# Performance work log

Hardware: AMD Instinct MI355X
Metric: run time of the kernel (lower is better)

## Reference

```python
import jax, jax.numpy as jnp
import numpy as np

EPS = 1e-08

def setup_inputs() -> dict:
    key = jax.random.key(0)
    kq, kk, kv = jax.random.split(key, 3)
    B, H, S, D = 2, 16, 2048, 64
    q = jax.random.normal(kq, (B, H, S, D), dtype=jnp.float32)
    k = jax.random.normal(kk, (B, H, S, D), dtype=jnp.float32)
    v = jax.random.normal(kv, (B, H, S, D), dtype=jnp.float32)
    return {"q": q, "k": k, "v": v}

def reference(q, k, v):
    d_k = q.shape[-1]
    # scores: [B,H,S,S]
    scores = jnp.einsum('bhqd,bhkd->bhqk', q, k) / jnp.sqrt(jnp.asarray(d_k, q.dtype))
    attn_weights = jax.nn.softmax(scores, axis=-1)
    # output: [B,H,S,D]
    output = jnp.einsum('bhqk,bhkd->bhqd', attn_weights, v)
    # non-differentiable row-norm preconditioner C_ii = 1/||A[i]||_2
    row_norms = jnp.linalg.norm(jax.lax.stop_gradient(output), axis=-1, keepdims=True)
    preconditioned_output = output / (row_norms + EPS)
    return (preconditioned_output, attn_weights)
```

## Files before the change

### kernel.cpp

```cpp
#include <hip/hip_runtime.h>

#define SS 2048
#define DD 64
#define S2 0.18033688011112042f

typedef __attribute__((ext_vector_type(4))) float f32x4;
typedef __attribute__((ext_vector_type(8))) short bfx8;
typedef __attribute__((ext_vector_type(4))) short bfx4;

__device__ __forceinline__ short f2bf(float f) {
    unsigned u = __builtin_bit_cast(unsigned, f);
    u += 0x7fffu + ((u >> 16) & 1u);
    return (short)(u >> 16);
}
__device__ __forceinline__ bfx8 pack8(f32x4 a, f32x4 b) {
    bfx8 r;
    r[0] = f2bf(a[0]); r[1] = f2bf(a[1]); r[2] = f2bf(a[2]); r[3] = f2bf(a[3]);
    r[4] = f2bf(b[0]); r[5] = f2bf(b[1]); r[6] = f2bf(b[2]); r[7] = f2bf(b[3]);
    return r;
}
__device__ __forceinline__ float bf2f(short s) {
    unsigned u = ((unsigned)(unsigned short)s) << 16;
    return __builtin_bit_cast(float, u);
}
__device__ __forceinline__ void bar_raw() {
    asm volatile("s_barrier" ::: "memory");
    __builtin_amdgcn_sched_barrier(0);
}
__device__ __forceinline__ void wait_vm0() {
    asm volatile("s_waitcnt vmcnt(0)" ::: "memory");
    __builtin_amdgcn_sched_barrier(0);
}
__device__ __forceinline__ void wait_vm2() {
    asm volatile("s_waitcnt vmcnt(2)" ::: "memory");
    __builtin_amdgcn_sched_barrier(0);
}
__device__ __forceinline__ void wait_vm8() {
    asm volatile("s_waitcnt vmcnt(8)" ::: "memory");
    __builtin_amdgcn_sched_barrier(0);
}
__device__ __forceinline__ void gload16(const void* g, void* l) {
    __builtin_amdgcn_global_load_lds(
        (const __attribute__((address_space(1))) unsigned*)g,
        (__attribute__((address_space(3))) unsigned*)l, 16, 0, 0);
}

__global__ __launch_bounds__(256) void prep_kernel(
    const float* __restrict__ k, const float* __restrict__ v,
    short* __restrict__ kbf, short* __restrict__ vtbf)
{
    const int blk = blockIdx.x;
    const int bh = blk >> 4, kc = blk & 15;
    const int tid = threadIdx.x;
    const long hoff = (long)bh * SS * DD;

    {
        const int key = tid >> 1, h = tid & 1;
        const float* kp = k + hoff + (long)(kc * 128 + key) * DD + h * 32;
        char* krow = (char*)kbf + ((long)bh * SS + kc * 128 + key) * 128;
        const int x = (key & 3) << 5;
        #pragma unroll
        for (int i = 0; i < 4; ++i) {
            f32x4 a = *(const f32x4*)(kp + i * 8);
            f32x4 b = *(const f32x4*)(kp + i * 8 + 4);
            *(bfx8*)(krow + ((h * 64 + i * 16) ^ x)) = pack8(a, b);
        }
    }

    __shared__ __align__(16) short Vl[64][136];
    {
        const int kq = (tid & 31) * 4, dg = (tid >> 5) * 8;
        const float* vp = v + hoff + (long)(kc * 128 + kq) * DD + dg;
        f32x4 r0a = *(const f32x4*)(vp),        r0b = *(const f32x4*)(vp + 4);
        f32x4 r1a = *(const f32x4*)(vp + DD),   r1b = *(const f32x4*)(vp + DD + 4);
        f32x4 r2a = *(const f32x4*)(vp + 2*DD), r2b = *(const f32x4*)(vp + 2*DD + 4);
        f32x4 r3a = *(const f32x4*)(vp + 3*DD), r3b = *(const f32x4*)(vp + 3*DD + 4);
        #pragma unroll
        for (int d = 0; d < 4; ++d) {
            bfx4 w;
            w[0] = f2bf(r0a[d]); w[1] = f2bf(r1a[d]);
            w[2] = f2bf(r2a[d]); w[3] = f2bf(r3a[d]);
            *(bfx4*)&Vl[dg + d][kq] = w;
        }
        #pragma unroll
        for (int d = 0; d < 4; ++d) {
            bfx4 w;
            w[0] = f2bf(r0b[d]); w[1] = f2bf(r1b[d]);
            w[2] = f2bf(r2b[d]); w[3] = f2bf(r3b[d]);
            *(bfx4*)&Vl[dg + 4 + d][kq] = w;
        }
    }
    __syncthreads();
    {
        const int d = tid >> 2, quar = tid & 3;
        char* vrow = (char*)vtbf + ((long)bh * 64 + d) * 4096 + kc * 256;
        const int x = (d & 3) << 5;
        #pragma unroll
        for (int i = 0; i < 4; ++i) {
            bfx8 w = *(const bfx8*)((const char*)&Vl[d][0] + quar * 64 + i * 16);
            *(bfx8*)(vrow + ((quar * 64 + i * 16) ^ x)) = w;
        }
    }
}

__global__ __launch_bounds__(256, 2) void pattn_main2(
    const float* __restrict__ q, const short* __restrict__ kbf,
    const short* __restrict__ vtbf, float* __restrict__ out,
    float* __restrict__ attn)
{
    const int blk = blockIdx.x;
    const int bh  = (blk & 7) * 4 + ((blk >> 3) & 3);
    const int qt  = blk >> 5;
    const int tid = threadIdx.x;
    const int wid = tid >> 6, lane = tid & 63;
    const int c = lane & 15, g = lane >> 4;

    __shared__ __align__(16) short Kl[2][64][64];
    __shared__ __align__(16) short Vt[2][64][64];
    __shared__ __align__(16) short Wc[4][32][80];

    const long hoff = (long)bh * SS * DD;
    const int  qA = qt * 128 + wid * 32 + c;
    const int  qB = qA + 16;

    bfx8 bqA0, bqA1, bqB0, bqB1;
    {
        const float* qp = q + hoff + (long)qA * DD + 8 * g;
        bqA0 = pack8(*(const f32x4*)(qp)      * S2, *(const f32x4*)(qp + 4)  * S2);
        bqA1 = pack8(*(const f32x4*)(qp + 32) * S2, *(const f32x4*)(qp + 36) * S2);
        const float* qp2 = q + hoff + (long)qB * DD + 8 * g;
        bqB0 = pack8(*(const f32x4*)(qp2)      * S2, *(const f32x4*)(qp2 + 4)  * S2);
        bqB1 = pack8(*(const f32x4*)(qp2 + 32) * S2, *(const f32x4*)(qp2 + 36) * S2);
    }

    const char* kb_base = (const char*)kbf + (long)bh * SS * 128;
    const char* vt_base = (const char*)vtbf + (long)bh * 64 * 4096;
    const int soff = wid * 2048 + lane * 16;

    auto issueK = [&](int kt, int b) {
        const char* gsrc = kb_base + (long)kt * 128 + soff;
        char* ldst = (char*)&Kl[b][0][0] + wid * 2048;
        gload16(gsrc, ldst);
        gload16(gsrc + 1024, ldst + 1024);
    };
    auto issueV = [&](int kt, int b) {
        #pragma unroll
        for (int j = 0; j < 2; ++j) {
            const int off = soff + j * 1024;
            const char* gsrc = vt_base + (long)(off >> 7) * 4096 + (long)kt * 2 + (off & 127);
            gload16(gsrc, (char*)&Vt[b][0][0] + wid * 2048 + j * 1024);
        }
    };

    float lsA[4] = {0.f,0.f,0.f,0.f}, lsB[4] = {0.f,0.f,0.f,0.f};
    issueK(0, 0);
    wait_vm0(); bar_raw();
    for (int it = 0; it < 32; ++it) {
        const int p = it & 1;
        issueK(((it + 1) & 31) * 64, p ^ 1);
        wait_vm2(); bar_raw();
        #pragma unroll
        for (int t = 0; t < 4; ++t) {
            const int row = t * 16 + c;
            const char* kr = (const char*)&Kl[p][row][0];
            const int x = (row & 3) << 5;
            bfx8 ka = *(const bfx8*)(kr + ((16 * g) ^ x));
            bfx8 kb = *(const bfx8*)(kr + ((64 + 16 * g) ^ x));
            f32x4 sA = {0.f,0.f,0.f,0.f}, sB = {0.f,0.f,0.f,0.f};
            sA = __builtin_amdgcn_mfma_f32_16x16x32_bf16(ka, bqA0, sA, 0, 0, 0);
            sA = __builtin_amdgcn_mfma_f32_16x16x32_bf16(kb, bqA1, sA, 0, 0, 0);
            sB = __builtin_amdgcn_mfma_f32_16x16x32_bf16(ka, bqB0, sB, 0, 0, 0);
            sB = __builtin_amdgcn_mfma_f32_16x16x32_bf16(kb, bqB1, sB, 0, 0, 0);
            #pragma unroll
            for (int r = 0; r < 4; ++r) {
                lsA[r] += __builtin_amdgcn_exp2f(sA[r]);
                lsB[r] += __builtin_amdgcn_exp2f(sB[r]);
            }
        }
        bar_raw();
    }
    float lsumA = (lsA[0] + lsA[1]) + (lsA[2] + lsA[3]);
    float lsumB = (lsB[0] + lsB[1]) + (lsB[2] + lsB[3]);
    lsumA += __shfl_xor(lsumA, 16, 64);
    lsumA += __shfl_xor(lsumA, 32, 64);
    lsumB += __shfl_xor(lsumB, 16, 64);
    lsumB += __shfl_xor(lsumB, 32, 64);
    const float invlA = 1.0f / lsumA;
    const float invlB = 1.0f / lsumB;

    f32x4 accA[4], accB[4];
    #pragma unroll
    for (int i = 0; i < 4; ++i) { accA[i] = (f32x4){0.f,0.f,0.f,0.f}; accB[i] = (f32x4){0.f,0.f,0.f,0.f}; }

    float* attnw = attn + (long)bh * SS * SS + (long)(qt * 128 + wid * 32) * SS;

    issueV(0, 0);
    wait_vm0(); bar_raw();
    for (int it = 0; it < 32; ++it) {
        const int p  = it & 1;
        const int k0 = it * 64;
        const int nk = ((it + 1) & 31) * 64;
        issueK(nk, p ^ 1);
        issueV(nk, p ^ 1);
        wait_vm8();
        bar_raw();

        #pragma unroll
        for (int half = 0; half < 2; ++half) {
            #pragma unroll
            for (int tt = 0; tt < 2; ++tt) {
                const int t = half * 2 + tt;
                const int row = t * 16 + c;
                const char* kr = (const char*)&Kl[p][row][0];
                const int x = (row & 3) << 5;
                bfx8 ka = *(const bfx8*)(kr + ((16 * g) ^ x));
                bfx8 kb = *(const bfx8*)(kr + ((64 + 16 * g) ^ x));
                f32x4 sA = {0.f,0.f,0.f,0.f}, sB = {0.f,0.f,0.f,0.f};
                sA = __builtin_amdgcn_mfma_f32_16x16x32_bf16(ka, bqA0, sA, 0, 0, 0);
                sA = __builtin_amdgcn_mfma_f32_16x16x32_bf16(kb, bqA1, sA, 0, 0, 0);
                sB = __builtin_amdgcn_mfma_f32_16x16x32_bf16(ka, bqB0, sB, 0, 0, 0);
                sB = __builtin_amdgcn_mfma_f32_16x16x32_bf16(kb, bqB1, sB, 0, 0, 0);
                bfx4 wpA, wpB;
                #pragma unroll
                for (int r = 0; r < 4; ++r) {
                    wpA[r] = f2bf(__builtin_amdgcn_exp2f(sA[r]) * invlA);
                    wpB[r] = f2bf(__builtin_amdgcn_exp2f(sB[r]) * invlB);
                }
                *(bfx4*)&Wc[wid][c][t * 16 + 4 * g]      = wpA;
                *(bfx4*)&Wc[wid][16 + c][t * 16 + 4 * g] = wpB;
            }
            bfx8 wbA = *(const bfx8*)((const char*)&Wc[wid][c][0]      + half * 64 + 16 * g);
            bfx8 wbB = *(const bfx8*)((const char*)&Wc[wid][16 + c][0] + half * 64 + 16 * g);
            #pragma unroll
            for (int ds = 0; ds < 4; ++ds) {
                const int vrow = ds * 16 + c;
                bfx8 va = *(const bfx8*)((const char*)&Vt[p][vrow][0] +
                                         ((half * 64 + 16 * g) ^ ((vrow & 3) << 5)));
                accA[ds] = __builtin_amdgcn_mfma_f32_16x16x32_bf16(va, wbA, accA[ds], 0, 0, 0);
                accB[ds] = __builtin_amdgcn_mfma_f32_16x16x32_bf16(va, wbB, accB[ds], 0, 0, 0);
            }
        }

        {
            const int col4 = c * 4;
            #pragma unroll
            for (int rg = 0; rg < 8; ++rg) {
                const int r = rg * 4 + g;
                bfx4 w4 = *(const bfx4*)&Wc[wid][r][col4];
                f32x4 o;
                o[0] = bf2f(w4[0]); o[1] = bf2f(w4[1]);
                o[2] = bf2f(w4[2]); o[3] = bf2f(w4[3]);
                __builtin_nontemporal_store(o, (f32x4*)(attnw + (long)r * SS + k0 + col4));
            }
        }
        bar_raw();
    }

    float ssqA = 0.f, ssqB = 0.f;
    #pragma unroll
    for (int ds = 0; ds < 4; ++ds)
        #pragma unroll
        for (int r = 0; r < 4; ++r) { ssqA += accA[ds][r] * accA[ds][r]; ssqB += accB[ds][r] * accB[ds][r]; }
    ssqA += __shfl_xor(ssqA, 16, 64);
    ssqA += __shfl_xor(ssqA, 32, 64);
    ssqB += __shfl_xor(ssqB, 16, 64);
    ssqB += __shfl_xor(ssqB, 32, 64);
    const float invA = 1.0f / (sqrtf(ssqA) + 1e-8f);
    const float invB = 1.0f / (sqrtf(ssqB) + 1e-8f);

    float* opA = out + hoff + (long)qA * DD;
    float* opB = out + hoff + (long)qB * DD;
    #pragma unroll
    for (int ds = 0; ds < 4; ++ds) {
        f32x4 oA, oB;
        #pragma unroll
        for (int r = 0; r < 4; ++r) { oA[r] = accA[ds][r] * invA; oB[r] = accB[ds][r] * invB; }
        *(f32x4*)&opA[ds * 16 + 4 * g] = oA;
        *(f32x4*)&opB[ds * 16 + 4 * g] = oB;
    }
}

__device__ __forceinline__ void fb_bar_lg() {
    asm volatile("s_waitcnt lgkmcnt(0)\n\ts_barrier" ::: "memory");
    __builtin_amdgcn_sched_barrier(0);
}
__global__ __launch_bounds__(256, 3) void pattn_fallback(
    const float* __restrict__ q, const float* __restrict__ k,
    const float* __restrict__ v, float* __restrict__ out,
    float* __restrict__ attn)
{
    const int blk = blockIdx.x;
    const int bh  = (blk & 7) * 4 + ((blk >> 3) & 3);
    const int qt  = blk >> 5;
    const int tid = threadIdx.x;
    const int wid = tid >> 6, lane = tid & 63;
    const int c = lane & 15, g = lane >> 4;

    const long hoff = (long)bh * SS * DD;
    const int  qrow = qt * 64 + wid * 16 + c;

    __shared__ __align__(16) short Kl[128][72];
    __shared__ __align__(16) short Vt[64][136];
    __shared__ __align__(16) short Wc[4][16][136];

    bfx8 bq0, bq1;
    {
        const float* qp = q + hoff + (long)qrow * DD + 8 * g;
        f32x4 x0 = *(const f32x4*)(qp)      * S2;
        f32x4 x1 = *(const f32x4*)(qp + 4)  * S2;
        f32x4 x2 = *(const f32x4*)(qp + 32) * S2;
        f32x4 x3 = *(const f32x4*)(qp + 36) * S2;
        bq0 = pack8(x0, x1);
        bq1 = pack8(x2, x3);
    }

    const int skey = tid >> 1, sdh = (tid & 1) << 5;
    const int vkq  = (tid & 31) * 4, vdg = (tid >> 5) * 8;
    f32x4 kr[8], vr[8];

    auto loadK = [&](int k0) {
        const float* kp = k + hoff + (long)(k0 + skey) * DD + sdh;
        #pragma unroll
        for (int i = 0; i < 8; ++i) kr[i] = *(const f32x4*)(kp + 4 * i);
    };
    auto writeK = [&]() {
        *(bfx8*)&Kl[skey][sdh + 0]  = pack8(kr[0], kr[1]);
        *(bfx8*)&Kl[skey][sdh + 8]  = pack8(kr[2], kr[3]);
        *(bfx8*)&Kl[skey][sdh + 16] = pack8(kr[4], kr[5]);
        *(bfx8*)&Kl[skey][sdh + 24] = pack8(kr[6], kr[7]);
    };
    auto loadV = [&](int k0) {
        const float* vp = v + hoff + (long)(k0 + vkq) * DD + vdg;
        #pragma unroll
        for (int r = 0; r < 4; ++r) {
            vr[2 * r]     = *(const f32x4*)(vp + r * DD);
            vr[2 * r + 1] = *(const f32x4*)(vp + r * DD + 4);
        }
    };
    auto writeV = [&]() {
        #pragma unroll
        for (int d = 0; d < 4; ++d) {
            bfx4 w;
            w[0] = f2bf(vr[0][d]); w[1] = f2bf(vr[2][d]);
            w[2] = f2bf(vr[4][d]); w[3] = f2bf(vr[6][d]);
            *(bfx4*)&Vt[vdg + d][vkq] = w;
        }
        #pragma unroll
        for (int d = 0; d < 4; ++d) {
            bfx4 w;
            w[0] = f2bf(vr[1][d]); w[1] = f2bf(vr[3][d]);
            w[2] = f2bf(vr[5][d]); w[3] = f2bf(vr[7][d]);
            *(bfx4*)&Vt[vdg + 4 + d][vkq] = w;
        }
    };

    float lsum = 0.f;
    loadK(0); wait_vm0(); writeK();
    for (int it = 0; it < 16; ++it) {
        fb_bar_lg();
        if (it < 15) loadK((it + 1) * 128);
        #pragma unroll
        for (int T = 0; T < 8; ++T) {
            bfx8 ka = *(const bfx8*)&Kl[T * 16 + c][8 * g];
            bfx8 kb = *(const bfx8*)&Kl[T * 16 + c][32 + 8 * g];
            f32x4 s = {0.f, 0.f, 0.f, 0.f};
            s = __builtin_amdgcn_mfma_f32_16x16x32_bf16(ka, bq0, s, 0, 0, 0);
            s = __builtin_amdgcn_mfma_f32_16x16x32_bf16(kb, bq1, s, 0, 0, 0);
            lsum += __builtin_amdgcn_exp2f(s[0]);
            lsum += __builtin_amdgcn_exp2f(s[1]);
            lsum += __builtin_amdgcn_exp2f(s[2]);
            lsum += __builtin_amdgcn_exp2f(s[3]);
        }
        if (it < 15) wait_vm0();
        bar_raw();
        if (it < 15) writeK();
    }
    lsum += __shfl_xor(lsum, 16, 64);
    lsum += __shfl_xor(lsum, 32, 64);
    const float invl = 1.0f / lsum;

    f32x4 acc[4];
    #pragma unroll
    for (int i = 0; i < 4; ++i) acc[i] = (f32x4){0.f, 0.f, 0.f, 0.f};

    float* attnw = attn + (long)bh * SS * SS + (long)(qt * 64 + wid * 16) * SS;

    loadK(0); loadV(0);
    wait_vm0();
    bar_raw();
    writeK(); writeV();
    for (int it = 0; it < 16; ++it) {
        const int k0 = it * 128;
        fb_bar_lg();
        if (it < 15) { loadK(k0 + 128); loadV(k0 + 128); }

        #pragma unroll
        for (int G = 0; G < 4; ++G) {
            #pragma unroll
            for (int t = 0; t < 2; ++t) {
                const int kb2 = G * 32 + t * 16;
                bfx8 ka = *(const bfx8*)&Kl[kb2 + c][8 * g];
                bfx8 kb = *(const bfx8*)&Kl[kb2 + c][32 + 8 * g];
                f32x4 s = {0.f, 0.f, 0.f, 0.f};
                s = __builtin_amdgcn_mfma_f32_16x16x32_bf16(ka, bq0, s, 0, 0, 0);
                s = __builtin_amdgcn_mfma_f32_16x16x32_bf16(kb, bq1, s, 0, 0, 0);
                bfx4 wp;
                wp[0] = f2bf(__builtin_amdgcn_exp2f(s[0]) * invl);
                wp[1] = f2bf(__builtin_amdgcn_exp2f(s[1]) * invl);
                wp[2] = f2bf(__builtin_amdgcn_exp2f(s[2]) * invl);
                wp[3] = f2bf(__builtin_amdgcn_exp2f(s[3]) * invl);
                *(bfx4*)&Wc[wid][c][kb2 + 4 * g] = wp;
            }
            bfx8 wb = *(const bfx8*)&Wc[wid][c][G * 32 + 8 * g];
            #pragma unroll
            for (int ds = 0; ds < 4; ++ds) {
                bfx8 va = *(const bfx8*)&Vt[ds * 16 + c][G * 32 + 8 * g];
                acc[ds] = __builtin_amdgcn_mfma_f32_16x16x32_bf16(va, wb, acc[ds], 0, 0, 0);
            }
        }

        {
            const int half = lane >> 5;
            const int col  = (lane & 31) * 4;
            #pragma unroll
            for (int rg = 0; rg < 8; ++rg) {
                const int r = rg * 2 + half;
                bfx4 w4 = *(const bfx4*)&Wc[wid][r][col];
                f32x4 o;
                o[0] = bf2f(w4[0]); o[1] = bf2f(w4[1]);
                o[2] = bf2f(w4[2]); o[3] = bf2f(w4[3]);
                __builtin_nontemporal_store(o, (f32x4*)(attnw + (long)r * SS + k0 + col));
            }
        }

        if (it < 15) {
            wait_vm8();
            bar_raw();
            writeK(); writeV();
        }
    }

    float ssq = 0.f;
    #pragma unroll
    for (int ds = 0; ds < 4; ++ds)
        #pragma unroll
        for (int r = 0; r < 4; ++r)
            ssq += acc[ds][r] * acc[ds][r];
    ssq += __shfl_xor(ssq, 16, 64);
    ssq += __shfl_xor(ssq, 32, 64);
    const float inv = 1.0f / (sqrtf(ssq) + 1e-8f);

    float* op = out + hoff + (long)qrow * DD;
    #pragma unroll
    for (int ds = 0; ds < 4; ++ds) {
        f32x4 o;
        o[0] = acc[ds][0] * inv; o[1] = acc[ds][1] * inv;
        o[2] = acc[ds][2] * inv; o[3] = acc[ds][3] * inv;
        *(f32x4*)&op[ds * 16 + 4 * g] = o;
    }
}

extern "C" void kernel_launch(void* const* d_in, const int* in_sizes, int n_in,
                              void* d_out, int out_size, void* d_ws, size_t ws_size,
                              hipStream_t stream) {
    const float* q = (const float*)d_in[0];
    const float* k = (const float*)d_in[1];
    const float* v = (const float*)d_in[2];
    float* out  = (float*)d_out;
    float* attn = out + (long)2 * 16 * SS * DD;

    const size_t need = 2UL * 32 * SS * DD * sizeof(short);
    if (ws_size >= need) {
        short* kbf  = (short*)d_ws;
        short* vtbf = kbf + (size_t)32 * SS * DD;
        hipLaunchKernelGGL(prep_kernel, dim3(512), dim3(256), 0, stream, k, v, kbf, vtbf);
        hipLaunchKernelGGL(pattn_main2, dim3(512), dim3(256), 0, stream, q, kbf, vtbf, out, attn);
    } else {
        hipLaunchKernelGGL(pattn_fallback, dim3(1024), dim3(256), 0, stream, q, k, v, out, attn);
    }
}
```

Before: 173.6 us.

## Deepen K prefetch ring and pool shared memory for higher occupancy

```diff
diff --git a/kernel.cpp b/kernel.cpp
--- a/kernel.cpp
+++ b/kernel.cpp
@@ -31,12 +31,16 @@
     asm volatile("s_waitcnt vmcnt(0)" ::: "memory");
     __builtin_amdgcn_sched_barrier(0);
 }
-__device__ __forceinline__ void wait_vm2() {
-    asm volatile("s_waitcnt vmcnt(2)" ::: "memory");
+__device__ __forceinline__ void wait_vm4() {
+    asm volatile("s_waitcnt vmcnt(4)" ::: "memory");
     __builtin_amdgcn_sched_barrier(0);
 }
 __device__ __forceinline__ void wait_vm8() {
     asm volatile("s_waitcnt vmcnt(8)" ::: "memory");
+    __builtin_amdgcn_sched_barrier(0);
+}
+__device__ __forceinline__ void wait_vm12() {
+    asm volatile("s_waitcnt vmcnt(12)" ::: "memory");
     __builtin_amdgcn_sched_barrier(0);
 }
 __device__ __forceinline__ void gload16(const void* g, void* l) {
@@ -103,7 +107,7 @@
     }
 }
 
-__global__ __launch_bounds__(256, 2) void pattn_main2(
+__global__ __launch_bounds__(256, 3) void pattn_main3(
     const float* __restrict__ q, const short* __restrict__ kbf,
     const short* __restrict__ vtbf, float* __restrict__ out,
     float* __restrict__ attn)
@@ -115,9 +119,8 @@
     const int wid = tid >> 6, lane = tid & 63;
     const int c = lane & 15, g = lane >> 4;
 
-    __shared__ __align__(16) short Kl[2][64][64];
-    __shared__ __align__(16) short Vt[2][64][64];
-    __shared__ __align__(16) short Wc[4][32][80];
+    __shared__ __align__(16) short pool[26624];
+    char* const P = (char*)pool;
 
     const long hoff = (long)bh * SS * DD;
     const int  qA = qt * 128 + wid * 32 + c;
@@ -137,9 +140,9 @@
     const char* vt_base = (const char*)vtbf + (long)bh * 64 * 4096;
     const int soff = wid * 2048 + lane * 16;
 
-    auto issueK = [&](int kt, int b) {
+    auto issueK = [&](int kt, int s) {
         const char* gsrc = kb_base + (long)kt * 128 + soff;
-        char* ldst = (char*)&Kl[b][0][0] + wid * 2048;
+        char* ldst = P + (s << 13) + wid * 2048;
         gload16(gsrc, ldst);
         gload16(gsrc + 1024, ldst + 1024);
     };
@@ -148,21 +151,22 @@
         for (int j = 0; j < 2; ++j) {
             const int off = soff + j * 1024;
             const char* gsrc = vt_base + (long)(off >> 7) * 4096 + (long)kt * 2 + (off & 127);
-            gload16(gsrc, (char*)&Vt[b][0][0] + wid * 2048 + j * 1024);
+            gload16(gsrc, P + ((2 + b) << 13) + wid * 2048 + j * 1024);
         }
     };
 
     float lsA[4] = {0.f,0.f,0.f,0.f}, lsB[4] = {0.f,0.f,0.f,0.f};
-    issueK(0, 0);
-    wait_vm0(); bar_raw();
+    issueK(0, 0); issueK(64, 1); issueK(128, 2);
     for (int it = 0; it < 32; ++it) {
-        const int p = it & 1;
-        issueK(((it + 1) & 31) * 64, p ^ 1);
-        wait_vm2(); bar_raw();
+        wait_vm4();
+        bar_raw();
+        if (it < 31) issueK(((it + 3) & 31) * 64, (it + 3) & 3);
+        __builtin_amdgcn_s_setprio(1);
+        const char* kbase = P + ((it & 3) << 13);
         #pragma unroll
         for (int t = 0; t < 4; ++t) {
             const int row = t * 16 + c;
-            const char* kr = (const char*)&Kl[p][row][0];
+            const char* kr = kbase + row * 128;
             const int x = (row & 3) << 5;
             bfx8 ka = *(const bfx8*)(kr + ((16 * g) ^ x));
             bfx8 kb = *(const bfx8*)(kr + ((64 + 16 * g) ^ x));
@@ -177,7 +181,7 @@
                 lsB[r] += __builtin_amdgcn_exp2f(sB[r]);
             }
         }
-        bar_raw();
+        __builtin_amdgcn_s_setprio(0);
     }
     float lsumA = (lsA[0] + lsA[1]) + (lsA[2] + lsA[3]);
     float lsumB = (lsB[0] + lsB[1]) + (lsB[2] + lsB[3]);
@@ -199,19 +203,27 @@
     for (int it = 0; it < 32; ++it) {
         const int p  = it & 1;
         const int k0 = it * 64;
-        const int nk = ((it + 1) & 31) * 64;
-        issueK(nk, p ^ 1);
-        issueV(nk, p ^ 1);
-        wait_vm8();
+        if (it == 0) {
+            issueV(64, 1);
+        } else {
+            const int nk = ((it + 1) & 31) * 64;
+            issueK(nk, p ^ 1);
+            issueV(nk, p ^ 1);
+        }
+        wait_vm12();
         bar_raw();
 
+        __builtin_amdgcn_s_setprio(1);
+        const char* kbase = P + (p << 13);
+        const char* vbase = P + ((2 + p) << 13);
+        char* const wcbase = P + 32768 + wid * 5120;
         #pragma unroll
         for (int half = 0; half < 2; ++half) {
             #pragma unroll
             for (int tt = 0; tt < 2; ++tt) {
                 const int t = half * 2 + tt;
                 const int row = t * 16 + c;
-                const char* kr = (const char*)&Kl[p][row][0];
+                const char* kr = kbase + row * 128;
                 const int x = (row & 3) << 5;
                 bfx8 ka = *(const bfx8*)(kr + ((16 * g) ^ x));
                 bfx8 kb = *(const bfx8*)(kr + ((64 + 16 * g) ^ x));
@@ -226,27 +238,28 @@
                     wpA[r] = f2bf(__builtin_amdgcn_exp2f(sA[r]) * invlA);
                     wpB[r] = f2bf(__builtin_amdgcn_exp2f(sB[r]) * invlB);
                 }
-                *(bfx4*)&Wc[wid][c][t * 16 + 4 * g]      = wpA;
-                *(bfx4*)&Wc[wid][16 + c][t * 16 + 4 * g] = wpB;
-            }
-            bfx8 wbA = *(const bfx8*)((const char*)&Wc[wid][c][0]      + half * 64 + 16 * g);
-            bfx8 wbB = *(const bfx8*)((const char*)&Wc[wid][16 + c][0] + half * 64 + 16 * g);
+                *(bfx4*)(wcbase + c * 160        + (t * 16 + 4 * g) * 2) = wpA;
+                *(bfx4*)(wcbase + (16 + c) * 160 + (t * 16 + 4 * g) * 2) = wpB;
+            }
+            bfx8 wbA = *(const bfx8*)(wcbase + c * 160        + half * 64 + 16 * g);
+            bfx8 wbB = *(const bfx8*)(wcbase + (16 + c) * 160 + half * 64 + 16 * g);
             #pragma unroll
             for (int ds = 0; ds < 4; ++ds) {
                 const int vrow = ds * 16 + c;
-                bfx8 va = *(const bfx8*)((const char*)&Vt[p][vrow][0] +
+                bfx8 va = *(const bfx8*)(vbase + vrow * 128 +
                                          ((half * 64 + 16 * g) ^ ((vrow & 3) << 5)));
                 accA[ds] = __builtin_amdgcn_mfma_f32_16x16x32_bf16(va, wbA, accA[ds], 0, 0, 0);
                 accB[ds] = __builtin_amdgcn_mfma_f32_16x16x32_bf16(va, wbB, accB[ds], 0, 0, 0);
             }
         }
+        __builtin_amdgcn_s_setprio(0);
 
         {
             const int col4 = c * 4;
             #pragma unroll
             for (int rg = 0; rg < 8; ++rg) {
                 const int r = rg * 4 + g;
-                bfx4 w4 = *(const bfx4*)&Wc[wid][r][col4];
+                bfx4 w4 = *(const bfx4*)(wcbase + r * 160 + col4 * 2);
                 f32x4 o;
                 o[0] = bf2f(w4[0]); o[1] = bf2f(w4[1]);
                 o[2] = bf2f(w4[2]); o[3] = bf2f(w4[3]);
@@ -474,7 +487,7 @@
         short* kbf  = (short*)d_ws;
         short* vtbf = kbf + (size_t)32 * SS * DD;
         hipLaunchKernelGGL(prep_kernel, dim3(512), dim3(256), 0, stream, k, v, kbf, vtbf);
-        hipLaunchKernelGGL(pattn_main2, dim3(512), dim3(256), 0, stream, q, kbf, vtbf, out, attn);
+        hipLaunchKernelGGL(pattn_main3, dim3(512), dim3(256), 0, stream, q, kbf, vtbf, out, attn);
     } else {
         hipLaunchKernelGGL(pattn_fallback, dim3(1024), dim3(256), 0, stream, q, k, v, out, attn);
     }
```

Measured after the change: 192.9 us. 1.11x slower.

## Load K and V tiles directly from global into registers, dropping LDS staging

Applied to the files above, without the earlier changes.

```diff
diff --git a/kernel.cpp b/kernel.cpp
--- a/kernel.cpp
+++ b/kernel.cpp
@@ -31,18 +31,9 @@
     asm volatile("s_waitcnt vmcnt(0)" ::: "memory");
     __builtin_amdgcn_sched_barrier(0);
 }
-__device__ __forceinline__ void wait_vm2() {
-    asm volatile("s_waitcnt vmcnt(2)" ::: "memory");
-    __builtin_amdgcn_sched_barrier(0);
-}
 __device__ __forceinline__ void wait_vm8() {
     asm volatile("s_waitcnt vmcnt(8)" ::: "memory");
     __builtin_amdgcn_sched_barrier(0);
-}
-__device__ __forceinline__ void gload16(const void* g, void* l) {
-    __builtin_amdgcn_global_load_lds(
-        (const __attribute__((address_space(1))) unsigned*)g,
-        (__attribute__((address_space(3))) unsigned*)l, 16, 0, 0);
 }
 
 __global__ __launch_bounds__(256) void prep_kernel(
@@ -50,20 +41,20 @@
     short* __restrict__ kbf, short* __restrict__ vtbf)
 {
     const int blk = blockIdx.x;
-    const int bh = blk >> 4, kc = blk & 15;
+    const int bh = (blk & 7) * 4 + ((blk >> 3) & 3);
+    const int kc = blk >> 5;
     const int tid = threadIdx.x;
     const long hoff = (long)bh * SS * DD;
 
     {
         const int key = tid >> 1, h = tid & 1;
         const float* kp = k + hoff + (long)(kc * 128 + key) * DD + h * 32;
-        char* krow = (char*)kbf + ((long)bh * SS + kc * 128 + key) * 128;
-        const int x = (key & 3) << 5;
+        char* krow = (char*)kbf + ((long)bh * SS + kc * 128 + key) * 128 + h * 64;
         #pragma unroll
         for (int i = 0; i < 4; ++i) {
             f32x4 a = *(const f32x4*)(kp + i * 8);
             f32x4 b = *(const f32x4*)(kp + i * 8 + 4);
-            *(bfx8*)(krow + ((h * 64 + i * 16) ^ x)) = pack8(a, b);
+            *(bfx8*)(krow + i * 16) = pack8(a, b);
         }
     }
 
@@ -93,17 +84,16 @@
     __syncthreads();
     {
         const int d = tid >> 2, quar = tid & 3;
-        char* vrow = (char*)vtbf + ((long)bh * 64 + d) * 4096 + kc * 256;
-        const int x = (d & 3) << 5;
+        char* vrow = (char*)vtbf + ((long)bh * 64 + d) * 4096 + kc * 256 + quar * 64;
         #pragma unroll
         for (int i = 0; i < 4; ++i) {
             bfx8 w = *(const bfx8*)((const char*)&Vl[d][0] + quar * 64 + i * 16);
-            *(bfx8*)(vrow + ((quar * 64 + i * 16) ^ x)) = w;
-        }
-    }
-}
-
-__global__ __launch_bounds__(256, 2) void pattn_main2(
+            *(bfx8*)(vrow + i * 16) = w;
+        }
+    }
+}
+
+__global__ __launch_bounds__(256) void pattn_nb(
     const float* __restrict__ q, const short* __restrict__ kbf,
     const short* __restrict__ vtbf, float* __restrict__ out,
     float* __restrict__ attn)
@@ -115,9 +105,7 @@
     const int wid = tid >> 6, lane = tid & 63;
     const int c = lane & 15, g = lane >> 4;
 
-    __shared__ __align__(16) short Kl[2][64][64];
-    __shared__ __align__(16) short Vt[2][64][64];
-    __shared__ __align__(16) short Wc[4][32][80];
+    __shared__ __align__(16) short Wc[4][32][84];
 
     const long hoff = (long)bh * SS * DD;
     const int  qA = qt * 128 + wid * 32 + c;
@@ -133,51 +121,37 @@
         bqB1 = pack8(*(const f32x4*)(qp2 + 32) * S2, *(const f32x4*)(qp2 + 36) * S2);
     }
 
-    const char* kb_base = (const char*)kbf + (long)bh * SS * 128;
-    const char* vt_base = (const char*)vtbf + (long)bh * 64 * 4096;
-    const int soff = wid * 2048 + lane * 16;
-
-    auto issueK = [&](int kt, int b) {
-        const char* gsrc = kb_base + (long)kt * 128 + soff;
-        char* ldst = (char*)&Kl[b][0][0] + wid * 2048;
-        gload16(gsrc, ldst);
-        gload16(gsrc + 1024, ldst + 1024);
-    };
-    auto issueV = [&](int kt, int b) {
-        #pragma unroll
-        for (int j = 0; j < 2; ++j) {
-            const int off = soff + j * 1024;
-            const char* gsrc = vt_base + (long)(off >> 7) * 4096 + (long)kt * 2 + (off & 127);
-            gload16(gsrc, (char*)&Vt[b][0][0] + wid * 2048 + j * 1024);
-        }
-    };
+    const char* kb = (const char*)kbf + (long)bh * SS * 128;
+    const char* vt = (const char*)vtbf + (long)bh * 64 * 4096;
+    const int koff = 16 * g;
 
     float lsA[4] = {0.f,0.f,0.f,0.f}, lsB[4] = {0.f,0.f,0.f,0.f};
-    issueK(0, 0);
-    wait_vm0(); bar_raw();
+    #pragma unroll 2
     for (int it = 0; it < 32; ++it) {
-        const int p = it & 1;
-        issueK(((it + 1) & 31) * 64, p ^ 1);
-        wait_vm2(); bar_raw();
+        const char* kt = kb + (long)it * 64 * 128;
+        bfx8 ka0 = *(const bfx8*)(kt + (0 * 16 + c) * 128 + koff);
+        bfx8 kv0 = *(const bfx8*)(kt + (0 * 16 + c) * 128 + 64 + koff);
+        bfx8 ka1 = *(const bfx8*)(kt + (1 * 16 + c) * 128 + koff);
+        bfx8 kv1 = *(const bfx8*)(kt + (1 * 16 + c) * 128 + 64 + koff);
+        bfx8 ka2 = *(const bfx8*)(kt + (2 * 16 + c) * 128 + koff);
+        bfx8 kv2 = *(const bfx8*)(kt + (2 * 16 + c) * 128 + 64 + koff);
+        bfx8 ka3 = *(const bfx8*)(kt + (3 * 16 + c) * 128 + koff);
+        bfx8 kv3 = *(const bfx8*)(kt + (3 * 16 + c) * 128 + 64 + koff);
         #pragma unroll
         for (int t = 0; t < 4; ++t) {
-            const int row = t * 16 + c;
-            const char* kr = (const char*)&Kl[p][row][0];
-            const int x = (row & 3) << 5;
-            bfx8 ka = *(const bfx8*)(kr + ((16 * g) ^ x));
-            bfx8 kb = *(const bfx8*)(kr + ((64 + 16 * g) ^ x));
+            bfx8 ka = (t == 0) ? ka0 : (t == 1) ? ka1 : (t == 2) ? ka2 : ka3;
+            bfx8 kv = (t == 0) ? kv0 : (t == 1) ? kv1 : (t == 2) ? kv2 : kv3;
             f32x4 sA = {0.f,0.f,0.f,0.f}, sB = {0.f,0.f,0.f,0.f};
             sA = __builtin_amdgcn_mfma_f32_16x16x32_bf16(ka, bqA0, sA, 0, 0, 0);
-            sA = __builtin_amdgcn_mfma_f32_16x16x32_bf16(kb, bqA1, sA, 0, 0, 0);
+            sA = __builtin_amdgcn_mfma_f32_16x16x32_bf16(kv, bqA1, sA, 0, 0, 0);
             sB = __builtin_amdgcn_mfma_f32_16x16x32_bf16(ka, bqB0, sB, 0, 0, 0);
-            sB = __builtin_amdgcn_mfma_f32_16x16x32_bf16(kb, bqB1, sB, 0, 0, 0);
+            sB = __builtin_amdgcn_mfma_f32_16x16x32_bf16(kv, bqB1, sB, 0, 0, 0);
             #pragma unroll
             for (int r = 0; r < 4; ++r) {
                 lsA[r] += __builtin_amdgcn_exp2f(sA[r]);
                 lsB[r] += __builtin_amdgcn_exp2f(sB[r]);
             }
         }
-        bar_raw();
     }
     float lsumA = (lsA[0] + lsA[1]) + (lsA[2] + lsA[3]);
     float lsumB = (lsB[0] + lsB[1]) + (lsB[2] + lsB[3]);
@@ -193,49 +167,46 @@
     for (int i = 0; i < 4; ++i) { accA[i] = (f32x4){0.f,0.f,0.f,0.f}; accB[i] = (f32x4){0.f,0.f,0.f,0.f}; }
 
     float* attnw = attn + (long)bh * SS * SS + (long)(qt * 128 + wid * 32) * SS;
-
-    issueV(0, 0);
-    wait_vm0(); bar_raw();
+    char* const wcb = (char*)&Wc[wid][0][0];
+
     for (int it = 0; it < 32; ++it) {
-        const int p  = it & 1;
-        const int k0 = it * 64;
-        const int nk = ((it + 1) & 31) * 64;
-        issueK(nk, p ^ 1);
-        issueV(nk, p ^ 1);
-        wait_vm8();
-        bar_raw();
+        const char* kt = kb + (long)it * 64 * 128;
+        bfx8 ka0 = *(const bfx8*)(kt + (0 * 16 + c) * 128 + koff);
+        bfx8 kv0 = *(const bfx8*)(kt + (0 * 16 + c) * 128 + 64 + koff);
+        bfx8 ka1 = *(const bfx8*)(kt + (1 * 16 + c) * 128 + koff);
+        bfx8 kv1 = *(const bfx8*)(kt + (1 * 16 + c) * 128 + 64 + koff);
+        bfx8 ka2 = *(const bfx8*)(kt + (2 * 16 + c) * 128 + koff);
+        bfx8 kv2 = *(const bfx8*)(kt + (2 * 16 + c) * 128 + 64 + koff);
+        bfx8 ka3 = *(const bfx8*)(kt + (3 * 16 + c) * 128 + koff);
+        bfx8 kv3 = *(const bfx8*)(kt + (3 * 16 + c) * 128 + 64 + koff);
 
         #pragma unroll
         for (int half = 0; half < 2; ++half) {
             #pragma unroll
             for (int tt = 0; tt < 2; ++tt) {
                 const int t = half * 2 + tt;
-                const int row = t * 16 + c;
-                const char* kr = (const char*)&Kl[p][row][0];
-                const int x = (row & 3) << 5;
-                bfx8 ka = *(const bfx8*)(kr + ((16 * g) ^ x));
-                bfx8 kb = *(const bfx8*)(kr + ((64 + 16 * g) ^ x));
+                bfx8 ka = (t == 0) ? ka0 : (t == 1) ? ka1 : (t == 2) ? ka2 : ka3;
+                bfx8 kv = (t == 0) ? kv0 : (t == 1) ? kv1 : (t == 2) ? kv2 : kv3;
                 f32x4 sA = {0.f,0.f,0.f,0.f}, sB = {0.f,0.f,0.f,0.f};
                 sA = __builtin_amdgcn_mfma_f32_16x16x32_bf16(ka, bqA0, sA, 0, 0, 0);
-                sA = __builtin_amdgcn_mfma_f32_16x16x32_bf16(kb, bqA1, sA, 0, 0, 0);
+                sA = __builtin_amdgcn_mfma_f32_16x16x32_bf16(kv, bqA1, sA, 0, 0, 0);
                 sB = __builtin_amdgcn_mfma_f32_16x16x32_bf16(ka, bqB0, sB, 0, 0, 0);
-                sB = __builtin_amdgcn_mfma_f32_16x16x32_bf16(kb, bqB1, sB, 0, 0, 0);
+                sB = __builtin_amdgcn_mfma_f32_16x16x32_bf16(kv, bqB1, sB, 0, 0, 0);
                 bfx4 wpA, wpB;
                 #pragma unroll
                 for (int r = 0; r < 4; ++r) {
                     wpA[r] = f2bf(__builtin_amdgcn_exp2f(sA[r]) * invlA);
                     wpB[r] = f2bf(__builtin_amdgcn_exp2f(sB[r]) * invlB);
                 }
-                *(bfx4*)&Wc[wid][c][t * 16 + 4 * g]      = wpA;
-                *(bfx4*)&Wc[wid][16 + c][t * 16 + 4 * g] = wpB;
-            }
-            bfx8 wbA = *(const bfx8*)((const char*)&Wc[wid][c][0]      + half * 64 + 16 * g);
-            bfx8 wbB = *(const bfx8*)((const char*)&Wc[wid][16 + c][0] + half * 64 + 16 * g);
+                *(bfx4*)(wcb + c * 168        + (t * 16 + 4 * g) * 2) = wpA;
+                *(bfx4*)(wcb + (16 + c) * 168 + (t * 16 + 4 * g) * 2) = wpB;
+            }
+            bfx8 wbA = *(const bfx8*)(wcb + c * 168        + half * 64 + 16 * g);
+            bfx8 wbB = *(const bfx8*)(wcb + (16 + c) * 168 + half * 64 + 16 * g);
             #pragma unroll
             for (int ds = 0; ds < 4; ++ds) {
-                const int vrow = ds * 16 + c;
-                bfx8 va = *(const bfx8*)((const char*)&Vt[p][vrow][0] +
-                                         ((half * 64 + 16 * g) ^ ((vrow & 3) << 5)));
+                const char* vr = vt + (long)(ds * 16 + c) * 4096 + it * 128 + half * 64 + 16 * g;
+                bfx8 va = *(const bfx8*)vr;
                 accA[ds] = __builtin_amdgcn_mfma_f32_16x16x32_bf16(va, wbA, accA[ds], 0, 0, 0);
                 accB[ds] = __builtin_amdgcn_mfma_f32_16x16x32_bf16(va, wbB, accB[ds], 0, 0, 0);
             }
@@ -246,14 +217,13 @@
             #pragma unroll
             for (int rg = 0; rg < 8; ++rg) {
                 const int r = rg * 4 + g;
-                bfx4 w4 = *(const bfx4*)&Wc[wid][r][col4];
+                bfx4 w4 = *(const bfx4*)(wcb + r * 168 + col4 * 2);
                 f32x4 o;
                 o[0] = bf2f(w4[0]); o[1] = bf2f(w4[1]);
                 o[2] = bf2f(w4[2]); o[3] = bf2f(w4[3]);
-                __builtin_nontemporal_store(o, (f32x4*)(attnw + (long)r * SS + k0 + col4));
-            }
-        }
-        bar_raw();
+                __builtin_nontemporal_store(o, (f32x4*)(attnw + (long)r * SS + it * 64 + col4));
+            }
+        }
     }
 
     float ssqA = 0.f, ssqB = 0.f;
@@ -474,7 +444,7 @@
         short* kbf  = (short*)d_ws;
         short* vtbf = kbf + (size_t)32 * SS * DD;
         hipLaunchKernelGGL(prep_kernel, dim3(512), dim3(256), 0, stream, k, v, kbf, vtbf);
-        hipLaunchKernelGGL(pattn_main2, dim3(512), dim3(256), 0, stream, q, kbf, vtbf, out, attn);
+        hipLaunchKernelGGL(pattn_nb, dim3(512), dim3(256), 0, stream, q, kbf, vtbf, out, attn);
     } else {
         hipLaunchKernelGGL(pattn_fallback, dim3(1024), dim3(256), 0, stream, q, k, v, out, attn);
     }
```

New measurement: 261.7 us. +50.7%, slower.
